# Performance work log

Measured on AMD Instinct MI355X. Metric: run time of the kernel, lower is better.

## Reference

```python
import jax, jax.numpy as jnp
import numpy as np
import math

B, S, H = 2, 2048, 1024
NH, HD = 16, 64  # num heads, head dim; NH*HD == H


def setup_inputs() -> dict:
    key = jax.random.key(0)
    k1, k2, k3 = jax.random.split(key, 3)
    hidden_states = jax.random.normal(k1, (B, S, H), dtype=jnp.float32)
    # causal multiplicative mask [1,1,S,S], 1.0 where attending is allowed
    mask = jnp.tril(jnp.ones((S, S), dtype=jnp.float32))[None, None]
    W_qkv = jax.random.normal(k2, (H, 3 * H), dtype=jnp.float32) * (1.0 / math.sqrt(H))
    b_qkv = jnp.zeros((3 * H,), dtype=jnp.float32)
    W_out = jax.random.normal(k3, (H, H), dtype=jnp.float32) * (1.0 / math.sqrt(H))
    b_out = jnp.zeros((H,), dtype=jnp.float32)
    return {"hidden_states": hidden_states, "mask": mask, "W_qkv": W_qkv,
            "b_qkv": b_qkv, "W_out": W_out, "b_out": b_out}


def reference(hidden_states, mask, W_qkv, b_qkv, W_out, b_out):
    b, s, h = hidden_states.shape
    # fused QKV projection then split into contiguous thirds (split_tensor_along_last_dim)
    qkv = jnp.einsum('bsh,hd->bsd', hidden_states, W_qkv) + b_qkv
    q, k, v = jnp.split(qkv, 3, axis=-1)
    # [b, s, nh*hd] -> [b, nh, s, hd]
    def to_heads(t):
        return t.reshape(b, s, NH, HD).transpose(0, 2, 1, 3)
    q, k, v = to_heads(q), to_heads(k), to_heads(v)
    q = q / jnp.sqrt(jnp.float32(HD))  # scaling_attention_score=True
    scores = jnp.einsum('bhqd,bhkd->bhqk', q, k)  # [b,nh,s,s]
    # multiplicative mask + large-negative bias trick from standard_attention
    scores = scores * mask - 10000.0 * (1.0 - mask)
    probs = jax.nn.softmax(scores, axis=-1)
    ctx = jnp.einsum('bhqk,bhkd->bhqd', probs, v)
    ctx = ctx.transpose(0, 2, 1, 3).reshape(b, s, h)  # [b, s, nh*hd]
    return jnp.einsum('bsh,hd->bsd', ctx, W_out) + b_out
```

## Files before the change

### kernel.cpp

```cpp
#include <hip/hip_runtime.h>
#include <cstdint>
#include <cstddef>

#define NHEAD 16
#define HDIM 64
#define SEQ 2048
#define BATCH 2
#define HID 1024

typedef __bf16 bf16x8 __attribute__((ext_vector_type(8)));
typedef float f32x4 __attribute__((ext_vector_type(4)));

__device__ __forceinline__ unsigned short f2bf(float f) {
    union { float f; unsigned u; } v; v.f = f;
    unsigned r = v.u + 0x7fffu + ((v.u >> 16) & 1u);
    return (unsigned short)(r >> 16);
}

__global__ __launch_bounds__(256) void convert_f32_bf16(
    const float* __restrict__ in, unsigned short* __restrict__ out, int n) {
    int i = (blockIdx.x * 256 + threadIdx.x) * 8;
    if (i >= n) return;
    float4 a = *(const float4*)(in + i);
    float4 b = *(const float4*)(in + i + 4);
    uint4 o;
    o.x = (unsigned)f2bf(a.x) | ((unsigned)f2bf(a.y) << 16);
    o.y = (unsigned)f2bf(a.z) | ((unsigned)f2bf(a.w) << 16);
    o.z = (unsigned)f2bf(b.x) | ((unsigned)f2bf(b.y) << 16);
    o.w = (unsigned)f2bf(b.z) | ((unsigned)f2bf(b.w) << 16);
    *(uint4*)(out + i) = o;
}

__global__ __launch_bounds__(256) void transpose_f32_bf16(
    const float* __restrict__ in, unsigned short* __restrict__ out, int R, int C) {
    __shared__ unsigned short T[64][72];
    int t = threadIdx.x;
    int c0 = blockIdx.x * 64, r0 = blockIdx.y * 64;
    for (int p = 0; p < 4; ++p) {
        int idx = (p * 256 + t) * 4;
        int row = idx >> 6, col = idx & 63;
        float4 v = *(const float4*)(in + (size_t)(r0 + row) * C + c0 + col);
        T[row][col + 0] = f2bf(v.x);
        T[row][col + 1] = f2bf(v.y);
        T[row][col + 2] = f2bf(v.z);
        T[row][col + 3] = f2bf(v.w);
    }
    __syncthreads();
    for (int p = 0; p < 4; ++p) {
        int idx = (p * 256 + t) * 4;
        int orow = idx >> 6, ocol = idx & 63;
        ushort4 u;
        u.x = T[ocol + 0][orow];
        u.y = T[ocol + 1][orow];
        u.z = T[ocol + 2][orow];
        u.w = T[ocol + 3][orow];
        *(ushort4*)(out + (size_t)(c0 + orow) * R + r0 + ocol) = u;
    }
}

__global__ __launch_bounds__(256) void transpose_v(
    const unsigned short* __restrict__ in, unsigned short* __restrict__ out) {
    __shared__ unsigned short T[64][72];
    int t = threadIdx.x;
    int s0 = blockIdx.x * 64, bh = blockIdx.y;
    const unsigned short* ip = in + (size_t)bh * SEQ * HDIM;
    unsigned short* op = out + (size_t)bh * HDIM * SEQ;
    for (int p = 0; p < 2; ++p) {
        int idx = (p * 256 + t) * 8;
        int row = idx >> 6, col = idx & 63;
        *(uint4*)&T[row][col] = *(const uint4*)(ip + (size_t)(s0 + row) * HDIM + col);
    }
    __syncthreads();
    for (int p = 0; p < 4; ++p) {
        int idx = (p * 256 + t) * 4;
        int d = idx >> 6, c = idx & 63;
        ushort4 u;
        u.x = T[c + 0][d];
        u.y = T[c + 1][d];
        u.z = T[c + 2][d];
        u.w = T[c + 3][d];
        *(ushort4*)(op + (size_t)d * SEQ + s0 + c) = u;
    }
}

#define GEMM_BODY(Aptr, Btptr, KDIM)                                                     \
    __shared__ unsigned short As[128][32];                                               \
    __shared__ unsigned short Bs[128][32];                                               \
    int t = threadIdx.x;                                                                 \
    int wave = t >> 6, lane = t & 63, ln = lane & 15, quad = lane >> 4;                  \
    int wm = wave >> 1, wn = wave & 1;                                                   \
    int m0 = blockIdx.y * 128, n0 = blockIdx.x * 128;                                    \
    int srow = lane >> 2, scol = (lane & 3) * 8;                                         \
    f32x4 zero4 = {0.f, 0.f, 0.f, 0.f};                                                  \
    f32x4 acc[4][4];                                                                     \
    for (int mi = 0; mi < 4; ++mi)                                                       \
        for (int ni = 0; ni < 4; ++ni) acc[mi][ni] = zero4;                              \
    for (int kt = 0; kt < (KDIM); kt += 32) {                                            \
        for (int p = 0; p < 2; ++p) {                                                    \
            int r0 = (wave * 2 + p) * 16 + srow;                                         \
            __builtin_amdgcn_global_load_lds(                                            \
                (const __attribute__((address_space(1))) void*)                          \
                    ((Aptr) + (size_t)(m0 + r0) * (KDIM) + kt + scol),                   \
                (__attribute__((address_space(3))) void*)&As[(wave * 2 + p) * 16][0],    \
                16, 0, 0);                                                               \
            __builtin_amdgcn_global_load_lds(                                            \
                (const __attribute__((address_space(1))) void*)                          \
                    ((Btptr) + (size_t)(n0 + r0) * (KDIM) + kt + scol),                  \
                (__attribute__((address_space(3))) void*)&Bs[(wave * 2 + p) * 16][0],    \
                16, 0, 0);                                                               \
        }                                                                                \
        __syncthreads();                                                                 \
        bf16x8 af[4], bfr[4];                                                            \
        for (int mi = 0; mi < 4; ++mi)                                                   \
            af[mi] = *(const bf16x8*)&As[wm * 64 + mi * 16 + ln][quad * 8];              \
        for (int ni = 0; ni < 4; ++ni)                                                   \
            bfr[ni] = *(const bf16x8*)&Bs[wn * 64 + ni * 16 + ln][quad * 8];             \
        for (int mi = 0; mi < 4; ++mi)                                                   \
            for (int ni = 0; ni < 4; ++ni)                                               \
                acc[mi][ni] = __builtin_amdgcn_mfma_f32_16x16x32_bf16(                   \
                    af[mi], bfr[ni], acc[mi][ni], 0, 0, 0);                              \
        __syncthreads();                                                                 \
    }

__global__ __launch_bounds__(256) void gemm_qkv(
    const unsigned short* __restrict__ A, const unsigned short* __restrict__ Bt,
    const float* __restrict__ bias,
    unsigned short* __restrict__ Qb, unsigned short* __restrict__ Kb,
    unsigned short* __restrict__ Vtmp) {
    GEMM_BODY(A, Bt, 1024)
    int nbase = n0 + wn * 64;
    for (int ni = 0; ni < 4; ++ni) {
        int gn = nbase + ni * 16 + ln;
        float bv = bias[gn];
        int third = gn >> 10;
        int rem = gn & 1023;
        int h = rem >> 6, d = rem & 63;
        unsigned short* dst = third == 0 ? Qb : (third == 1 ? Kb : Vtmp);
        float scale = third == 0 ? 0.1803368801111f : 1.0f;
        for (int mi = 0; mi < 4; ++mi) {
            for (int r = 0; r < 4; ++r) {
                int gm = m0 + wm * 64 + mi * 16 + quad * 4 + r;
                int b = gm >> 11, s = gm & 2047;
                size_t bh = (size_t)(b * NHEAD + h);
                dst[(bh * SEQ + s) * HDIM + d] = f2bf((acc[mi][ni][r] + bv) * scale);
            }
        }
    }
}

__global__ __launch_bounds__(256) void gemm_out(
    const unsigned short* __restrict__ A, const unsigned short* __restrict__ Bt,
    const float* __restrict__ bias, float* __restrict__ C) {
    GEMM_BODY(A, Bt, 1024)
    int nbase = n0 + wn * 64;
    for (int ni = 0; ni < 4; ++ni) {
        int gn = nbase + ni * 16 + ln;
        float bv = bias[gn];
        for (int mi = 0; mi < 4; ++mi) {
            for (int r = 0; r < 4; ++r) {
                int gm = m0 + wm * 64 + mi * 16 + quad * 4 + r;
                C[(size_t)gm * HID + gn] = acc[mi][ni][r] + bv;
            }
        }
    }
}

__global__ __launch_bounds__(256) void flash_attn(
    const unsigned short* __restrict__ Qb, const unsigned short* __restrict__ Kb,
    const unsigned short* __restrict__ Vt, unsigned short* __restrict__ Ctx) {
    __shared__ unsigned short KsB[2][64][64];
    __shared__ unsigned short VsB[2][64][64];
    __shared__ unsigned short Ps[4][16][72];
    int tid = threadIdx.x;
    int wave = tid >> 6, lane = tid & 63, ln = lane & 15, quad = lane >> 4;
    int bx = blockIdx.x, bh = blockIdx.y;
    int qiA = bx;
    int q0A = qiA * 64, q0B = (31 - bx) * 64;
    const size_t baseQK = (size_t)bh * SEQ * HDIM;
    const size_t baseV = (size_t)bh * HDIM * SEQ;
    int b = bh >> 4, h = bh & 15;

    int rIn = lane >> 3;
    int gsw = ((lane & 7) ^ rIn) * 8;

    bf16x8 aqA0, aqA1, aqB0, aqB1;
    {
        const unsigned short* qp =
            Qb + baseQK + (size_t)(q0A + wave * 16 + ln) * HDIM + quad * 8;
        aqA0 = *(const bf16x8*)qp;
        aqA1 = *(const bf16x8*)(qp + 32);
        qp = Qb + baseQK + (size_t)(q0B + wave * 16 + ln) * HDIM + quad * 8;
        aqB0 = *(const bf16x8*)qp;
        aqB1 = *(const bf16x8*)(qp + 32);
    }
    bf16x8 aqc0 = aqA0, aqc1 = aqA1;

    auto prefetch = [&](int kj, int bi) {
        const unsigned short* kb = Kb + baseQK + (size_t)kj * 64 * HDIM;
        const unsigned short* vb = Vt + baseV + kj * 64;
        for (int c = wave; c < 8; c += 4) {
            __builtin_amdgcn_global_load_lds(
                (const __attribute__((address_space(1))) void*)(kb + (c * 8 + rIn) * HDIM + gsw),
                (__attribute__((address_space(3))) void*)&KsB[bi][c * 8][0], 16, 0, 0);
            __builtin_amdgcn_global_load_lds(
                (const __attribute__((address_space(1))) void*)(vb + (size_t)(c * 8 + rIn) * SEQ + gsw),
                (__attribute__((address_space(3))) void*)&VsB[bi][c * 8][0], 16, 0, 0);
        }
    };

    f32x4 zero4 = {0.f, 0.f, 0.f, 0.f};
    f32x4 o[4];
    float lacc = 0.f;
    for (int i = 0; i < 4; ++i) o[i] = zero4;

    prefetch(0, 0);
    for (int t = 0; t <= 32; ++t) {
        __syncthreads();
        if (t < 32) {
            int kn = (t + 1 <= qiA) ? (t + 1) : (t - qiA);
            prefetch(kn, (t + 1) & 1);
        }
        int buf = t & 1;
        bool diag = (t == qiA) || (t == 32);

        f32x4 s4[4];
        for (int ni = 0; ni < 4; ++ni) s4[ni] = zero4;
        for (int kk = 0; kk < 2; ++kk) {
            bf16x8 bq = kk ? aqc1 : aqc0;
            for (int ni = 0; ni < 4; ++ni) {
                bf16x8 ak = *(const bf16x8*)
                    &KsB[buf][ni * 16 + ln][(((kk * 4 + quad)) ^ (ln & 7)) * 8];
                s4[ni] = __builtin_amdgcn_mfma_f32_16x16x32_bf16(ak, bq, s4[ni], 0, 0, 0);
            }
        }
        if (diag) {
            for (int ni = 0; ni < 4; ++ni)
                for (int r = 0; r < 4; ++r)
                    if (ni * 16 + quad * 4 + r > wave * 16 + ln) s4[ni][r] = -1.0e38f;
        }

        for (int ni = 0; ni < 4; ++ni) {
            float e0 = __builtin_amdgcn_exp2f(s4[ni][0]);
            float e1 = __builtin_amdgcn_exp2f(s4[ni][1]);
            float e2 = __builtin_amdgcn_exp2f(s4[ni][2]);
            float e3 = __builtin_amdgcn_exp2f(s4[ni][3]);
            lacc += (e0 + e1) + (e2 + e3);
            ushort4 pk;
            pk.x = f2bf(e0); pk.y = f2bf(e1); pk.z = f2bf(e2); pk.w = f2bf(e3);
            *(ushort4*)&Ps[wave][ln][ni * 16 + quad * 4] = pk;
        }

        for (int kk = 0; kk < 2; ++kk) {
            bf16x8 bp = *(const bf16x8*)&Ps[wave][ln][kk * 32 + quad * 8];
            for (int ni = 0; ni < 4; ++ni) {
                bf16x8 av = *(const bf16x8*)
                    &VsB[buf][ni * 16 + ln][(((kk * 4 + quad)) ^ (ln & 7)) * 8];
                o[ni] = __builtin_amdgcn_mfma_f32_16x16x32_bf16(av, bp, o[ni], 0, 0, 0);
            }
        }

        if (diag) {
            float sum = lacc;
            sum += __shfl_xor(sum, 16);
            sum += __shfl_xor(sum, 32);
            float linv = __builtin_amdgcn_rcpf(sum);
            int q0 = (t == 32) ? q0B : q0A;
            size_t rowb = ((size_t)(b * SEQ + q0 + wave * 16 + ln)) * HID + h * 64;
            for (int ni = 0; ni < 4; ++ni) {
                ushort4 u;
                u.x = f2bf(o[ni][0] * linv);
                u.y = f2bf(o[ni][1] * linv);
                u.z = f2bf(o[ni][2] * linv);
                u.w = f2bf(o[ni][3] * linv);
                *(ushort4*)&Ctx[rowb + ni * 16 + quad * 4] = u;
            }
            for (int i = 0; i < 4; ++i) o[i] = zero4;
            lacc = 0.f;
            aqc0 = aqB0;
            aqc1 = aqB1;
        }
    }
}

extern "C" void kernel_launch(void* const* d_in, const int* in_sizes, int n_in,
                              void* d_out, int out_size, void* d_ws, size_t ws_size,
                              hipStream_t stream) {
    const float* X = (const float*)d_in[0];
    const float* Wqkv = (const float*)d_in[2];
    const float* bqkv = (const float*)d_in[3];
    const float* Wout = (const float*)d_in[4];
    const float* bout = (const float*)d_in[5];
    float* out = (float*)d_out;

    char* ws = (char*)d_ws;
    unsigned short* Xb   = (unsigned short*)(ws + 0);
    unsigned short* Vt   = (unsigned short*)(ws + 0);
    unsigned short* W1t  = (unsigned short*)(ws + 8388608);
    unsigned short* W2t  = (unsigned short*)(ws + 14680064);
    unsigned short* Qb   = (unsigned short*)(ws + 16777216);
    unsigned short* Kb   = (unsigned short*)(ws + 25165824);
    unsigned short* Vtmp = (unsigned short*)(ws + 33554432);
    unsigned short* Ctx  = (unsigned short*)(ws + 41943040);

    convert_f32_bf16<<<2048, 256, 0, stream>>>(X, Xb, 4194304);
    transpose_f32_bf16<<<dim3(48, 16), 256, 0, stream>>>(Wqkv, W1t, 1024, 3072);
    transpose_f32_bf16<<<dim3(16, 16), 256, 0, stream>>>(Wout, W2t, 1024, 1024);
    gemm_qkv<<<dim3(24, 32), 256, 0, stream>>>(Xb, W1t, bqkv, Qb, Kb, Vtmp);
    transpose_v<<<dim3(32, 32), 256, 0, stream>>>(Vtmp, Vt);
    flash_attn<<<dim3(16, 32), 256, 0, stream>>>(Qb, Kb, Vt, Ctx);
    gemm_out<<<dim3(8, 32), 256, 0, stream>>>(Ctx, W2t, bout, out);
}
```

Measured before the change: 208.6 us.

## Fuse V transpose into QKV GEMM, share K/V tiles across paired query blocks

The QKV GEMM epilogue now writes V directly in transposed layout with packed stores, which removes the separate transpose_v kernel and its extra round trip through global memory. The flash attention kernel now walks one K/V sweep for both paired query tiles, reusing each loaded tile for the A and B queries instead of loading tiles twice. It also alternates pairing order by head. The output GEMM uses 64-row tiles so the grid has twice as many blocks, and bf16 conversion uses the hardware packed-convert builtin. Risks include higher register pressure from two accumulator sets in attention and a different rounding path in the packed conversion.

```diff
diff --git a/kernel.cpp b/kernel.cpp
--- a/kernel.cpp
+++ b/kernel.cpp
@@ -9,12 +9,22 @@
 #define HID 1024
 
 typedef __bf16 bf16x8 __attribute__((ext_vector_type(8)));
+typedef __bf16 bf16x2_t __attribute__((ext_vector_type(2)));
 typedef float f32x4 __attribute__((ext_vector_type(4)));
 
 __device__ __forceinline__ unsigned short f2bf(float f) {
     union { float f; unsigned u; } v; v.f = f;
     unsigned r = v.u + 0x7fffu + ((v.u >> 16) & 1u);
     return (unsigned short)(r >> 16);
+}
+
+__device__ __forceinline__ unsigned pk_bf16(float a, float b) {
+#if __has_builtin(__builtin_amdgcn_cvt_pk_bf16_f32)
+    bf16x2_t p = __builtin_amdgcn_cvt_pk_bf16_f32(a, b);
+    return __builtin_bit_cast(unsigned, p);
+#else
+    return (unsigned)f2bf(a) | ((unsigned)f2bf(b) << 16);
+#endif
 }
 
 __global__ __launch_bounds__(256) void convert_f32_bf16(
@@ -24,10 +34,10 @@
     float4 a = *(const float4*)(in + i);
     float4 b = *(const float4*)(in + i + 4);
     uint4 o;
-    o.x = (unsigned)f2bf(a.x) | ((unsigned)f2bf(a.y) << 16);
-    o.y = (unsigned)f2bf(a.z) | ((unsigned)f2bf(a.w) << 16);
-    o.z = (unsigned)f2bf(b.x) | ((unsigned)f2bf(b.y) << 16);
-    o.w = (unsigned)f2bf(b.z) | ((unsigned)f2bf(b.w) << 16);
+    o.x = pk_bf16(a.x, a.y);
+    o.y = pk_bf16(a.z, a.w);
+    o.z = pk_bf16(b.x, b.y);
+    o.w = pk_bf16(b.z, b.w);
     *(uint4*)(out + i) = o;
 }
 
@@ -55,31 +65,6 @@
         u.z = T[ocol + 2][orow];
         u.w = T[ocol + 3][orow];
         *(ushort4*)(out + (size_t)(c0 + orow) * R + r0 + ocol) = u;
-    }
-}
-
-__global__ __launch_bounds__(256) void transpose_v(
-    const unsigned short* __restrict__ in, unsigned short* __restrict__ out) {
-    __shared__ unsigned short T[64][72];
-    int t = threadIdx.x;
-    int s0 = blockIdx.x * 64, bh = blockIdx.y;
-    const unsigned short* ip = in + (size_t)bh * SEQ * HDIM;
-    unsigned short* op = out + (size_t)bh * HDIM * SEQ;
-    for (int p = 0; p < 2; ++p) {
-        int idx = (p * 256 + t) * 8;
-        int row = idx >> 6, col = idx & 63;
-        *(uint4*)&T[row][col] = *(const uint4*)(ip + (size_t)(s0 + row) * HDIM + col);
-    }
-    __syncthreads();
-    for (int p = 0; p < 4; ++p) {
-        int idx = (p * 256 + t) * 4;
-        int d = idx >> 6, c = idx & 63;
-        ushort4 u;
-        u.x = T[c + 0][d];
-        u.y = T[c + 1][d];
-        u.z = T[c + 2][d];
-        u.w = T[c + 3][d];
-        *(ushort4*)(op + (size_t)d * SEQ + s0 + c) = u;
     }
 }
 
@@ -126,7 +111,7 @@
     const unsigned short* __restrict__ A, const unsigned short* __restrict__ Bt,
     const float* __restrict__ bias,
     unsigned short* __restrict__ Qb, unsigned short* __restrict__ Kb,
-    unsigned short* __restrict__ Vtmp) {
+    unsigned short* __restrict__ Vt) {
     GEMM_BODY(A, Bt, 1024)
     int nbase = n0 + wn * 64;
     for (int ni = 0; ni < 4; ++ni) {
@@ -135,14 +120,26 @@
         int third = gn >> 10;
         int rem = gn & 1023;
         int h = rem >> 6, d = rem & 63;
-        unsigned short* dst = third == 0 ? Qb : (third == 1 ? Kb : Vtmp);
-        float scale = third == 0 ? 0.1803368801111f : 1.0f;
-        for (int mi = 0; mi < 4; ++mi) {
-            for (int r = 0; r < 4; ++r) {
-                int gm = m0 + wm * 64 + mi * 16 + quad * 4 + r;
-                int b = gm >> 11, s = gm & 2047;
+        if (third == 2) {
+            for (int mi = 0; mi < 4; ++mi) {
+                int gm0 = m0 + wm * 64 + mi * 16 + quad * 4;
+                int b = gm0 >> 11, s = gm0 & 2047;
                 size_t bh = (size_t)(b * NHEAD + h);
-                dst[(bh * SEQ + s) * HDIM + d] = f2bf((acc[mi][ni][r] + bv) * scale);
+                uint2 u;
+                u.x = pk_bf16(acc[mi][ni][0] + bv, acc[mi][ni][1] + bv);
+                u.y = pk_bf16(acc[mi][ni][2] + bv, acc[mi][ni][3] + bv);
+                *(uint2*)&Vt[(bh * HDIM + d) * SEQ + s] = u;
+            }
+        } else {
+            unsigned short* dst = third == 0 ? Qb : Kb;
+            float scale = third == 0 ? 0.1803368801111f : 1.0f;
+            for (int mi = 0; mi < 4; ++mi) {
+                for (int r = 0; r < 4; ++r) {
+                    int gm = m0 + wm * 64 + mi * 16 + quad * 4 + r;
+                    int b = gm >> 11, s = gm & 2047;
+                    size_t bh = (size_t)(b * NHEAD + h);
+                    dst[(bh * SEQ + s) * HDIM + d] = f2bf((acc[mi][ni][r] + bv) * scale);
+                }
             }
         }
     }
@@ -151,14 +148,50 @@
 __global__ __launch_bounds__(256) void gemm_out(
     const unsigned short* __restrict__ A, const unsigned short* __restrict__ Bt,
     const float* __restrict__ bias, float* __restrict__ C) {
-    GEMM_BODY(A, Bt, 1024)
-    int nbase = n0 + wn * 64;
+    __shared__ unsigned short As[64][32];
+    __shared__ unsigned short Bs[128][32];
+    int t = threadIdx.x;
+    int wave = t >> 6, lane = t & 63, ln = lane & 15, quad = lane >> 4;
+    int wm = wave >> 1, wn = wave & 1;
+    int m0 = blockIdx.y * 64, n0 = blockIdx.x * 128;
+    int srow = lane >> 2, scol = (lane & 3) * 8;
+    f32x4 zero4 = {0.f, 0.f, 0.f, 0.f};
+    f32x4 acc[2][4];
+    for (int mi = 0; mi < 2; ++mi)
+        for (int ni = 0; ni < 4; ++ni) acc[mi][ni] = zero4;
+    for (int kt = 0; kt < 1024; kt += 32) {
+        for (int c = wave * 3; c < wave * 3 + 3; ++c) {
+            if (c < 4) {
+                __builtin_amdgcn_global_load_lds(
+                    (const __attribute__((address_space(1))) void*)
+                        (A + (size_t)(m0 + c * 16 + srow) * 1024 + kt + scol),
+                    (__attribute__((address_space(3))) void*)&As[c * 16][0], 16, 0, 0);
+            } else {
+                int cb = c - 4;
+                __builtin_amdgcn_global_load_lds(
+                    (const __attribute__((address_space(1))) void*)
+                        (Bt + (size_t)(n0 + cb * 16 + srow) * 1024 + kt + scol),
+                    (__attribute__((address_space(3))) void*)&Bs[cb * 16][0], 16, 0, 0);
+            }
+        }
+        __syncthreads();
+        bf16x8 af[2], bfr[4];
+        for (int mi = 0; mi < 2; ++mi)
+            af[mi] = *(const bf16x8*)&As[wm * 32 + mi * 16 + ln][quad * 8];
+        for (int ni = 0; ni < 4; ++ni)
+            bfr[ni] = *(const bf16x8*)&Bs[wn * 64 + ni * 16 + ln][quad * 8];
+        for (int mi = 0; mi < 2; ++mi)
+            for (int ni = 0; ni < 4; ++ni)
+                acc[mi][ni] = __builtin_amdgcn_mfma_f32_16x16x32_bf16(
+                    af[mi], bfr[ni], acc[mi][ni], 0, 0, 0);
+        __syncthreads();
+    }
     for (int ni = 0; ni < 4; ++ni) {
-        int gn = nbase + ni * 16 + ln;
+        int gn = n0 + wn * 64 + ni * 16 + ln;
         float bv = bias[gn];
-        for (int mi = 0; mi < 4; ++mi) {
+        for (int mi = 0; mi < 2; ++mi) {
             for (int r = 0; r < 4; ++r) {
-                int gm = m0 + wm * 64 + mi * 16 + quad * 4 + r;
+                int gm = m0 + wm * 32 + mi * 16 + quad * 4 + r;
                 C[(size_t)gm * HID + gn] = acc[mi][ni][r] + bv;
             }
         }
@@ -173,9 +206,10 @@
     __shared__ unsigned short Ps[4][16][72];
     int tid = threadIdx.x;
     int wave = tid >> 6, lane = tid & 63, ln = lane & 15, quad = lane >> 4;
-    int bx = blockIdx.x, bh = blockIdx.y;
-    int qiA = bx;
-    int q0A = qiA * 64, q0B = (31 - bx) * 64;
+    int bh = blockIdx.y;
+    int qiA = (bh < 16) ? blockIdx.x : (15 - blockIdx.x);
+    int qiB = 31 - qiA;
+    int q0A = qiA * 64, q0B = qiB * 64;
     const size_t baseQK = (size_t)bh * SEQ * HDIM;
     const size_t baseV = (size_t)bh * HDIM * SEQ;
     int b = bh >> 4, h = bh & 15;
@@ -193,7 +227,6 @@
         aqB0 = *(const bf16x8*)qp;
         aqB1 = *(const bf16x8*)(qp + 32);
     }
-    bf16x8 aqc0 = aqA0, aqc1 = aqA1;
 
     auto prefetch = [&](int kj, int bi) {
         const unsigned short* kb = Kb + baseQK + (size_t)kj * 64 * HDIM;
@@ -209,77 +242,106 @@
     };
 
     f32x4 zero4 = {0.f, 0.f, 0.f, 0.f};
-    f32x4 o[4];
-    float lacc = 0.f;
-    for (int i = 0; i < 4; ++i) o[i] = zero4;
+    f32x4 oA[4], oB[4];
+    float laccA = 0.f, laccB = 0.f;
+    for (int i = 0; i < 4; ++i) { oA[i] = zero4; oB[i] = zero4; }
+
+    auto epilogue = [&](f32x4* o, float lacc, int q0) {
+        float sum = lacc;
+        sum += __shfl_xor(sum, 16);
+        sum += __shfl_xor(sum, 32);
+        float linv = __builtin_amdgcn_rcpf(sum);
+        size_t rowb = ((size_t)(b * SEQ + q0 + wave * 16 + ln)) * HID + h * 64;
+        for (int ni = 0; ni < 4; ++ni) {
+            uint2 u;
+            u.x = pk_bf16(o[ni][0] * linv, o[ni][1] * linv);
+            u.y = pk_bf16(o[ni][2] * linv, o[ni][3] * linv);
+            *(uint2*)&Ctx[rowb + ni * 16 + quad * 4] = u;
+        }
+    };
 
     prefetch(0, 0);
-    for (int t = 0; t <= 32; ++t) {
+    for (int k = 0; k <= qiB; ++k) {
         __syncthreads();
-        if (t < 32) {
-            int kn = (t + 1 <= qiA) ? (t + 1) : (t - qiA);
-            prefetch(kn, (t + 1) & 1);
-        }
-        int buf = t & 1;
-        bool diag = (t == qiA) || (t == 32);
-
-        f32x4 s4[4];
-        for (int ni = 0; ni < 4; ++ni) s4[ni] = zero4;
-        for (int kk = 0; kk < 2; ++kk) {
-            bf16x8 bq = kk ? aqc1 : aqc0;
+        if (k < qiB) prefetch(k + 1, (k + 1) & 1);
+        int buf = k & 1;
+
+        {
+            f32x4 s4[4];
+            for (int ni = 0; ni < 4; ++ni) s4[ni] = zero4;
+            for (int kk = 0; kk < 2; ++kk) {
+                bf16x8 bq = kk ? aqB1 : aqB0;
+                for (int ni = 0; ni < 4; ++ni) {
+                    bf16x8 ak = *(const bf16x8*)
+                        &KsB[buf][ni * 16 + ln][((kk * 4 + quad) ^ (ln & 7)) * 8];
+                    s4[ni] = __builtin_amdgcn_mfma_f32_16x16x32_bf16(ak, bq, s4[ni], 0, 0, 0);
+                }
+            }
+            if (k == qiB) {
+                for (int ni = 0; ni < 4; ++ni)
+                    for (int r = 0; r < 4; ++r)
+                        if (ni * 16 + quad * 4 + r > wave * 16 + ln) s4[ni][r] = -1.0e38f;
+            }
             for (int ni = 0; ni < 4; ++ni) {
-                bf16x8 ak = *(const bf16x8*)
-                    &KsB[buf][ni * 16 + ln][(((kk * 4 + quad)) ^ (ln & 7)) * 8];
-                s4[ni] = __builtin_amdgcn_mfma_f32_16x16x32_bf16(ak, bq, s4[ni], 0, 0, 0);
-            }
-        }
-        if (diag) {
-            for (int ni = 0; ni < 4; ++ni)
-                for (int r = 0; r < 4; ++r)
-                    if (ni * 16 + quad * 4 + r > wave * 16 + ln) s4[ni][r] = -1.0e38f;
-        }
-
-        for (int ni = 0; ni < 4; ++ni) {
-            float e0 = __builtin_amdgcn_exp2f(s4[ni][0]);
-            float e1 = __builtin_amdgcn_exp2f(s4[ni][1]);
-            float e2 = __builtin_amdgcn_exp2f(s4[ni][2]);
-            float e3 = __builtin_amdgcn_exp2f(s4[ni][3]);
-            lacc += (e0 + e1) + (e2 + e3);
-            ushort4 pk;
-            pk.x = f2bf(e0); pk.y = f2bf(e1); pk.z = f2bf(e2); pk.w = f2bf(e3);
-            *(ushort4*)&Ps[wave][ln][ni * 16 + quad * 4] = pk;
-        }
-
-        for (int kk = 0; kk < 2; ++kk) {
-            bf16x8 bp = *(const bf16x8*)&Ps[wave][ln][kk * 32 + quad * 8];
+                float e0 = __builtin_amdgcn_exp2f(s4[ni][0]);
+                float e1 = __builtin_amdgcn_exp2f(s4[ni][1]);
+                float e2 = __builtin_amdgcn_exp2f(s4[ni][2]);
+                float e3 = __builtin_amdgcn_exp2f(s4[ni][3]);
+                laccB += (e0 + e1) + (e2 + e3);
+                uint2 pk;
+                pk.x = pk_bf16(e0, e1);
+                pk.y = pk_bf16(e2, e3);
+                *(uint2*)&Ps[wave][ln][ni * 16 + quad * 4] = pk;
+            }
+            for (int kk = 0; kk < 2; ++kk) {
+                bf16x8 bp = *(const bf16x8*)&Ps[wave][ln][kk * 32 + quad * 8];
+                for (int ni = 0; ni < 4; ++ni) {
+                    bf16x8 av = *(const bf16x8*)
+                        &VsB[buf][ni * 16 + ln][((kk * 4 + quad) ^ (ln & 7)) * 8];
+                    oB[ni] = __builtin_amdgcn_mfma_f32_16x16x32_bf16(av, bp, oB[ni], 0, 0, 0);
+                }
+            }
+        }
+
+        if (k <= qiA) {
+            f32x4 s4[4];
+            for (int ni = 0; ni < 4; ++ni) s4[ni] = zero4;
+            for (int kk = 0; kk < 2; ++kk) {
+                bf16x8 bq = kk ? aqA1 : aqA0;
+                for (int ni = 0; ni < 4; ++ni) {
+                    bf16x8 ak = *(const bf16x8*)
+                        &KsB[buf][ni * 16 + ln][((kk * 4 + quad) ^ (ln & 7)) * 8];
+                    s4[ni] = __builtin_amdgcn_mfma_f32_16x16x32_bf16(ak, bq, s4[ni], 0, 0, 0);
+                }
+            }
+            if (k == qiA) {
+                for (int ni = 0; ni < 4; ++ni)
+                    for (int r = 0; r < 4; ++r)
+                        if (ni * 16 + quad * 4 + r > wave * 16 + ln) s4[ni][r] = -1.0e38f;
+            }
             for (int ni = 0; ni < 4; ++ni) {
-                bf16x8 av = *(const bf16x8*)
-                    &VsB[buf][ni * 16 + ln][(((kk * 4 + quad)) ^ (ln & 7)) * 8];
-                o[ni] = __builtin_amdgcn_mfma_f32_16x16x32_bf16(av, bp, o[ni], 0, 0, 0);
-            }
-        }
-
-        if (diag) {
-            float sum = lacc;
-            sum += __shfl_xor(sum, 16);
-            sum += __shfl_xor(sum, 32);
-            float linv = __builtin_amdgcn_rcpf(sum);
-            int q0 = (t == 32) ? q0B : q0A;
-            size_t rowb = ((size_t)(b * SEQ + q0 + wave * 16 + ln)) * HID + h * 64;
-            for (int ni = 0; ni < 4; ++ni) {
-                ushort4 u;
-                u.x = f2bf(o[ni][0] * linv);
-                u.y = f2bf(o[ni][1] * linv);
-                u.z = f2bf(o[ni][2] * linv);
-                u.w = f2bf(o[ni][3] * linv);
-                *(ushort4*)&Ctx[rowb + ni * 16 + quad * 4] = u;
-            }
-            for (int i = 0; i < 4; ++i) o[i] = zero4;
-            lacc = 0.f;
-            aqc0 = aqB0;
-            aqc1 = aqB1;
-        }
-    }
+                float e0 = __builtin_amdgcn_exp2f(s4[ni][0]);
+                float e1 = __builtin_amdgcn_exp2f(s4[ni][1]);
+                float e2 = __builtin_amdgcn_exp2f(s4[ni][2]);
+                float e3 = __builtin_amdgcn_exp2f(s4[ni][3]);
+                laccA += (e0 + e1) + (e2 + e3);
+                uint2 pk;
+                pk.x = pk_bf16(e0, e1);
+                pk.y = pk_bf16(e2, e3);
+                *(uint2*)&Ps[wave][ln][ni * 16 + quad * 4] = pk;
+            }
+            for (int kk = 0; kk < 2; ++kk) {
+                bf16x8 bp = *(const bf16x8*)&Ps[wave][ln][kk * 32 + quad * 8];
+                for (int ni = 0; ni < 4; ++ni) {
+                    bf16x8 av = *(const bf16x8*)
+                        &VsB[buf][ni * 16 + ln][((kk * 4 + quad) ^ (ln & 7)) * 8];
+                    oA[ni] = __builtin_amdgcn_mfma_f32_16x16x32_bf16(av, bp, oA[ni], 0, 0, 0);
+                }
+            }
+            if (k == qiA) epilogue(oA, laccA, q0A);
+        }
+    }
+    epilogue(oB, laccB, q0B);
 }
 
 extern "C" void kernel_launch(void* const* d_in, const int* in_sizes, int n_in,
@@ -293,20 +355,18 @@
     float* out = (float*)d_out;
 
     char* ws = (char*)d_ws;
-    unsigned short* Xb   = (unsigned short*)(ws + 0);
-    unsigned short* Vt   = (unsigned short*)(ws + 0);
-    unsigned short* W1t  = (unsigned short*)(ws + 8388608);
-    unsigned short* W2t  = (unsigned short*)(ws + 14680064);
-    unsigned short* Qb   = (unsigned short*)(ws + 16777216);
-    unsigned short* Kb   = (unsigned short*)(ws + 25165824);
-    unsigned short* Vtmp = (unsigned short*)(ws + 33554432);
-    unsigned short* Ctx  = (unsigned short*)(ws + 41943040);
+    unsigned short* Xb  = (unsigned short*)(ws + 0);
+    unsigned short* W1t = (unsigned short*)(ws + 8388608);
+    unsigned short* W2t = (unsigned short*)(ws + 14680064);
+    unsigned short* Qb  = (unsigned short*)(ws + 16777216);
+    unsigned short* Kb  = (unsigned short*)(ws + 25165824);
+    unsigned short* Vt  = (unsigned short*)(ws + 33554432);
+    unsigned short* Ctx = (unsigned short*)(ws + 41943040);
 
     convert_f32_bf16<<<2048, 256, 0, stream>>>(X, Xb, 4194304);
     transpose_f32_bf16<<<dim3(48, 16), 256, 0, stream>>>(Wqkv, W1t, 1024, 3072);
     transpose_f32_bf16<<<dim3(16, 16), 256, 0, stream>>>(Wout, W2t, 1024, 1024);
-    gemm_qkv<<<dim3(24, 32), 256, 0, stream>>>(Xb, W1t, bqkv, Qb, Kb, Vtmp);
-    transpose_v<<<dim3(32, 32), 256, 0, stream>>>(Vtmp, Vt);
+    gemm_qkv<<<dim3(24, 32), 256, 0, stream>>>(Xb, W1t, bqkv, Qb, Kb, Vt);
     flash_attn<<<dim3(16, 32), 256, 0, stream>>>(Qb, Kb, Vt, Ctx);
-    gemm_out<<<dim3(8, 32), 256, 0, stream>>>(Ctx, W2t, bout, out);
-}
+    gemm_out<<<dim3(8, 64), 256, 0, stream>>>(Ctx, W2t, bout, out);
+}
```

New measurement: 212.9 us. 2.1% more time.
